# Optimization experiments

Hardware: AMD Instinct MI355X
Metric: run time of the kernel (lower is better)

The kernel has to match this reference:

```python
import jax, jax.numpy as jnp
import numpy as np

EMBED_DIM = 128
WINDOW_SIZE = 128
B, S, D = 2, 2048, EMBED_DIM
NEG_INF = -1e9


def setup_inputs() -> dict:
    key = jax.random.key(0)
    kq, kk, kv = jax.random.split(key, 3)
    q = jax.random.normal(kq, (B, S, D), dtype=jnp.float32)
    k = jax.random.normal(kk, (B, S, D), dtype=jnp.float32)
    v = jax.random.normal(kv, (B, S, D), dtype=jnp.float32)
    return {"q": q, "k": k, "v": v}


def reference(q, k, v):
    # Sliding-window causal attention: token i attends to [i-W, i] inclusive.
    Bq, Sq, Dq = q.shape
    W = WINDOW_SIZE
    scale = Dq ** -0.5
    offsets = jnp.arange(-W, 1)                      # [W+1]
    idx = jnp.arange(Sq)[:, None] + offsets[None, :]  # [S, W+1]
    valid = idx >= 0                                  # mask out-of-range (pre-sequence) keys
    idx_c = jnp.clip(idx, 0, Sq - 1)
    k_win = k[:, idx_c]                               # [B, S, W+1, D]
    v_win = v[:, idx_c]                               # [B, S, W+1, D]
    scores = jnp.einsum('bsd,bswd->bsw', q, k_win) * scale
    scores = jnp.where(valid[None, :, :], scores, NEG_INF)
    attn = jax.nn.softmax(scores, axis=-1)            # [B, S, W+1]
    out = jnp.einsum('bsw,bswd->bsd', attn, v_win)    # [B, S, D]
    return out
```

## Files before the change

### kernel.cpp

```cpp
#include <hip/hip_runtime.h>
#include <math.h>

#define SEQ 2048
#define DIME 128
#define BQ 16
#define NEG_INF -1.0e9f

typedef __attribute__((ext_vector_type(8))) short bf16x8;
typedef __attribute__((ext_vector_type(4))) float f32x4;

static __device__ __forceinline__ short f2b(float x) {
  union { float f; unsigned u; } v; v.f = x;
  unsigned r = v.u + 0x7FFF + ((v.u >> 16) & 1);
  return (short)(r >> 16);
}

static __device__ __forceinline__ bf16x8 pack8(const float4 lo, const float4 hi) {
  bf16x8 f;
  f[0] = f2b(lo.x); f[1] = f2b(lo.y); f[2] = f2b(lo.z); f[3] = f2b(lo.w);
  f[4] = f2b(hi.x); f[5] = f2b(hi.y); f[6] = f2b(hi.z); f[7] = f2b(hi.w);
  return f;
}

__global__ __launch_bounds__(256) void swa_kernel(
    const float* __restrict__ q, const float* __restrict__ k,
    const float* __restrict__ v, float* __restrict__ out) {
  __shared__ float P[160][18];
  __shared__ float mW[9][16];
  __shared__ float sW[9][16];
  __shared__ float scaleW[10][16];

  const int tid = threadIdx.x;
  const int lane = tid & 63;
  const int w = tid >> 6;
  const int col = lane & 15;
  const int g = lane >> 4;

  const int blk = blockIdx.x;
  const int b = blk >> 7;
  const int qs = (blk & 127) * BQ;
  const int kbase = qs - 128;

  const float* __restrict__ qb = q + (size_t)b * SEQ * DIME;
  const float* __restrict__ kb = k + (size_t)b * SEQ * DIME;
  const float* __restrict__ vb = v + (size_t)b * SEQ * DIME;

  float4 qlo[4], qhi[4];
  {
    const float* qrow = qb + (size_t)(qs + col) * DIME + 8 * g;
#pragma unroll
    for (int kc = 0; kc < 4; ++kc) {
      qlo[kc] = *(const float4*)(qrow + 32 * kc);
      qhi[kc] = *(const float4*)(qrow + 32 * kc + 4);
    }
  }

  float4 kraw[3][8];
#pragma unroll
  for (int ti = 0; ti < 2; ++ti) {
    const int t = 2 * w + ti;
    int krow = kbase + 16 * t + col;
    krow = krow < 0 ? 0 : krow;
    const float* krp = kb + (size_t)krow * DIME + 8 * g;
#pragma unroll
    for (int kc = 0; kc < 4; ++kc) {
      kraw[ti][2 * kc]     = *(const float4*)(krp + 32 * kc);
      kraw[ti][2 * kc + 1] = *(const float4*)(krp + 32 * kc + 4);
    }
  }
  if (w == 0) {
    int krow = kbase + 16 * 8 + col;
    const float* krp = kb + (size_t)krow * DIME + 8 * g;
#pragma unroll
    for (int kc = 0; kc < 4; ++kc) {
      kraw[2][2 * kc]     = *(const float4*)(krp + 32 * kc);
      kraw[2][2 * kc + 1] = *(const float4*)(krp + 32 * kc + 4);
    }
  }

  bf16x8 qf[4];
#pragma unroll
  for (int kc = 0; kc < 4; ++kc) qf[kc] = pack8(qlo[kc], qhi[kc]);

  float2 vv[5][8];
#pragma unroll
  for (int c = 0; c < 5; ++c)
#pragma unroll
    for (int j = 0; j < 8; ++j) {
      int kg = kbase + 32 * c + 8 * g + j;
      kg = kg < 0 ? 0 : (kg > SEQ - 1 ? SEQ - 1 : kg);
      vv[c][j] = *(const float2*)(vb + (size_t)kg * DIME + 32 * w + 2 * col);
    }

  P[144 + (tid >> 4)][tid & 15] = 0.f;

  const float scale = 0.08838834764831845f;
  auto process = [&](int t, const float4 (&raw)[8]) {
    f32x4 acc = {0.f, 0.f, 0.f, 0.f};
#pragma unroll
    for (int kc = 0; kc < 4; ++kc)
      acc = __builtin_amdgcn_mfma_f32_16x16x32_bf16(
          pack8(raw[2 * kc], raw[2 * kc + 1]), qf[kc], acc, 0, 0, 0);
    float sc[4];
    float m = NEG_INF;
#pragma unroll
    for (int r = 0; r < 4; ++r) {
      const int kg = kbase + 16 * t + 4 * g + r;
      const int qg = qs + col;
      const bool valid = (kg >= 0) && (kg >= qg - 128) && (kg <= qg);
      sc[r] = valid ? acc[r] * scale : NEG_INF;
      m = fmaxf(m, sc[r]);
    }
    m = fmaxf(m, __shfl_xor(m, 16));
    m = fmaxf(m, __shfl_xor(m, 32));
    float s = 0.f;
#pragma unroll
    for (int r = 0; r < 4; ++r) { sc[r] = __expf(sc[r] - m); s += sc[r]; }
    s += __shfl_xor(s, 16);
    s += __shfl_xor(s, 32);
    if (g == 0) { mW[t][col] = m; sW[t][col] = s; }
#pragma unroll
    for (int r = 0; r < 4; ++r) P[16 * t + 4 * g + r][col] = sc[r];
  };
  process(2 * w, kraw[0]);
  process(2 * w + 1, kraw[1]);
  if (w == 0) process(8, kraw[2]);

  __syncthreads();

  if (tid < 160) {
    const int t = tid >> 4, qq = tid & 15;
    if (t == 9) {
      scaleW[9][qq] = 0.f;
    } else {
      float M = mW[0][qq];
#pragma unroll
      for (int t2 = 1; t2 < 9; ++t2) M = fmaxf(M, mW[t2][qq]);
      float St = 0.f;
#pragma unroll
      for (int t2 = 0; t2 < 9; ++t2) St += sW[t2][qq] * __expf(mW[t2][qq] - M);
      scaleW[t][qq] = __expf(mW[t][qq] - M) / St;
    }
  }
  __syncthreads();

  f32x4 o0 = {0.f, 0.f, 0.f, 0.f}, o1 = {0.f, 0.f, 0.f, 0.f};
#pragma unroll
  for (int c = 0; c < 5; ++c) {
    const float sw = scaleW[2 * c + (g >> 1)][col];
    bf16x8 pa, b0, b1;
#pragma unroll
    for (int j = 0; j < 8; ++j) {
      pa[j] = f2b(P[32 * c + 8 * g + j][col] * sw);
      b0[j] = f2b(vv[c][j].x);
      b1[j] = f2b(vv[c][j].y);
    }
    o0 = __builtin_amdgcn_mfma_f32_16x16x32_bf16(pa, b0, o0, 0, 0, 0);
    o1 = __builtin_amdgcn_mfma_f32_16x16x32_bf16(pa, b1, o1, 0, 0, 0);
  }

#pragma unroll
  for (int r = 0; r < 4; ++r) {
    const int qrow = 4 * g + r;
    float2 val = {o0[r], o1[r]};
    *(float2*)&out[(size_t)(b * SEQ + qs + qrow) * DIME + 32 * w + 2 * col] = val;
  }
}

extern "C" void kernel_launch(void* const* d_in, const int* in_sizes, int n_in,
                              void* d_out, int out_size, void* d_ws, size_t ws_size,
                              hipStream_t stream) {
  const float* q = (const float*)d_in[0];
  const float* k = (const float*)d_in[1];
  const float* v = (const float*)d_in[2];
  float* out = (float*)d_out;
  dim3 grid(256), block(256);
  swa_kernel<<<grid, block, 0, stream>>>(q, k, v, out);
}
```

Before: 13.34 us.

## Split output head dimension across two blocks and compute softmax scale per thread

```diff
diff --git a/kernel.cpp b/kernel.cpp
--- a/kernel.cpp
+++ b/kernel.cpp
@@ -28,7 +28,6 @@
   __shared__ float P[160][18];
   __shared__ float mW[9][16];
   __shared__ float sW[9][16];
-  __shared__ float scaleW[10][16];
 
   const int tid = threadIdx.x;
   const int lane = tid & 63;
@@ -37,8 +36,10 @@
   const int g = lane >> 4;
 
   const int blk = blockIdx.x;
-  const int b = blk >> 7;
-  const int qs = (blk & 127) * BQ;
+  const int h = blk >> 8;
+  const int tile = blk & 255;
+  const int b = tile >> 7;
+  const int qs = (tile & 127) * BQ;
   const int kbase = qs - 128;
 
   const float* __restrict__ qb = q + (size_t)b * SEQ * DIME;
@@ -69,7 +70,7 @@
     }
   }
   if (w == 0) {
-    int krow = kbase + 16 * 8 + col;
+    const int krow = kbase + 16 * 8 + col;
     const float* krp = kb + (size_t)krow * DIME + 8 * g;
 #pragma unroll
     for (int kc = 0; kc < 4; ++kc) {
@@ -78,19 +79,19 @@
     }
   }
 
-  bf16x8 qf[4];
-#pragma unroll
-  for (int kc = 0; kc < 4; ++kc) qf[kc] = pack8(qlo[kc], qhi[kc]);
-
-  float2 vv[5][8];
+  float vvf[5][8];
 #pragma unroll
   for (int c = 0; c < 5; ++c)
 #pragma unroll
     for (int j = 0; j < 8; ++j) {
       int kg = kbase + 32 * c + 8 * g + j;
       kg = kg < 0 ? 0 : (kg > SEQ - 1 ? SEQ - 1 : kg);
-      vv[c][j] = *(const float2*)(vb + (size_t)kg * DIME + 32 * w + 2 * col);
+      vvf[c][j] = vb[(size_t)kg * DIME + 64 * h + 16 * w + col];
     }
+
+  bf16x8 qf[4];
+#pragma unroll
+  for (int kc = 0; kc < 4; ++kc) qf[kc] = pack8(qlo[kc], qhi[kc]);
 
   P[144 + (tid >> 4)][tid & 15] = 0.f;
 
@@ -128,42 +129,39 @@
 
   __syncthreads();
 
-  if (tid < 160) {
-    const int t = tid >> 4, qq = tid & 15;
-    if (t == 9) {
-      scaleW[9][qq] = 0.f;
-    } else {
-      float M = mW[0][qq];
+  float M = mW[0][col];
 #pragma unroll
-      for (int t2 = 1; t2 < 9; ++t2) M = fmaxf(M, mW[t2][qq]);
-      float St = 0.f;
+  for (int t = 1; t < 9; ++t) M = fmaxf(M, mW[t][col]);
+  float e[9], St = 0.f;
 #pragma unroll
-      for (int t2 = 0; t2 < 9; ++t2) St += sW[t2][qq] * __expf(mW[t2][qq] - M);
-      scaleW[t][qq] = __expf(mW[t][qq] - M) / St;
-    }
+  for (int t = 0; t < 9; ++t) {
+    e[t] = __expf(mW[t][col] - M);
+    St += sW[t][col] * e[t];
   }
-  __syncthreads();
-
-  f32x4 o0 = {0.f, 0.f, 0.f, 0.f}, o1 = {0.f, 0.f, 0.f, 0.f};
+  const float inv = 1.0f / St;
+  float swt[5];
 #pragma unroll
   for (int c = 0; c < 5; ++c) {
-    const float sw = scaleW[2 * c + (g >> 1)][col];
-    bf16x8 pa, b0, b1;
+    const float ehi = (2 * c + 1 < 9) ? e[2 * c + 1] : 0.f;
+    swt[c] = ((g >> 1) ? ehi : e[2 * c]) * inv;
+  }
+
+  f32x4 o = {0.f, 0.f, 0.f, 0.f};
+#pragma unroll
+  for (int c = 0; c < 5; ++c) {
+    bf16x8 pa, bv;
 #pragma unroll
     for (int j = 0; j < 8; ++j) {
-      pa[j] = f2b(P[32 * c + 8 * g + j][col] * sw);
-      b0[j] = f2b(vv[c][j].x);
-      b1[j] = f2b(vv[c][j].y);
+      pa[j] = f2b(P[32 * c + 8 * g + j][col] * swt[c]);
+      bv[j] = f2b(vvf[c][j]);
     }
-    o0 = __builtin_amdgcn_mfma_f32_16x16x32_bf16(pa, b0, o0, 0, 0, 0);
-    o1 = __builtin_amdgcn_mfma_f32_16x16x32_bf16(pa, b1, o1, 0, 0, 0);
+    o = __builtin_amdgcn_mfma_f32_16x16x32_bf16(pa, bv, o, 0, 0, 0);
   }
 
 #pragma unroll
   for (int r = 0; r < 4; ++r) {
     const int qrow = 4 * g + r;
-    float2 val = {o0[r], o1[r]};
-    *(float2*)&out[(size_t)(b * SEQ + qs + qrow) * DIME + 32 * w + 2 * col] = val;
+    out[(size_t)(b * SEQ + qs + qrow) * DIME + 64 * h + 16 * w + col] = o[r];
   }
 }
 
@@ -174,6 +172,6 @@
   const float* k = (const float*)d_in[1];
   const float* v = (const float*)d_in[2];
   float* out = (float*)d_out;
-  dim3 grid(256), block(256);
+  dim3 grid(512), block(256);
   swa_kernel<<<grid, block, 0, stream>>>(q, k, v, out);
 }
```

After: 15.83 us. 18.6% more time.
